# Performance work log

Measured on AMD Instinct MI355X. Metric: run time of the kernel, lower is better.

Reference implementation:

```python
import jax, jax.numpy as jnp
import numpy as np

NUM_HEADS = 8
NUM_GROUPS = 32
EPS = 1e-5


def setup_inputs() -> dict:
    key = jax.random.key(0)
    ks = jax.random.split(key, 6)
    C = 512
    scale = 1.0 / np.sqrt(C)
    return {
        "q": jax.random.normal(ks[0], (2, C, 64, 64), dtype=jnp.float32),
        "gn_w": jnp.ones((C,), jnp.float32),
        "gn_b": jnp.zeros((C,), jnp.float32),
        "wq": jax.random.normal(ks[1], (C, C), jnp.float32) * scale,
        "bq": jnp.zeros((C,), jnp.float32),
        "wk": jax.random.normal(ks[2], (C, C), jnp.float32) * scale,
        "bk": jnp.zeros((C,), jnp.float32),
        "wv": jax.random.normal(ks[3], (C, C), jnp.float32) * scale,
        "bv": jnp.zeros((C,), jnp.float32),
        "wo": jax.random.normal(ks[4], (C, C), jnp.float32) * scale,
        "bo": jnp.zeros((C,), jnp.float32),
    }


def _group_norm(x, w, b):
    # x: [B, C, H, W]
    B, C, H, W = x.shape
    xg = x.reshape(B, NUM_GROUPS, C // NUM_GROUPS, H, W)
    mean = xg.mean(axis=(2, 3, 4), keepdims=True)
    var = xg.var(axis=(2, 3, 4), keepdims=True)
    xn = ((xg - mean) * jax.lax.rsqrt(var + EPS)).reshape(B, C, H, W)
    return xn * w[None, :, None, None] + b[None, :, None, None]


def reference(q, gn_w, gn_b, wq, bq, wk, bk, wv, bv, wo, bo):
    B, C, H, W = q.shape
    hd = C // NUM_HEADS
    resid = q
    x = _group_norm(q, gn_w, gn_b)
    x = x.reshape(B, C, H * W).transpose(0, 2, 1)  # [B, N, C]
    # torch Linear: y = x @ W.T + b  (self-attention: k = v = x)
    qp = x @ wq.T + bq
    kp = x @ wk.T + bk
    vp = x @ wv.T + bv
    N = H * W
    def split(t):  # [B, N, C] -> [B, h, N, hd]
        return t.reshape(B, N, NUM_HEADS, hd).transpose(0, 2, 1, 3)
    qh, kh, vh = split(qp), split(kp), split(vp)
    scores = jnp.einsum('bhnc,bhmc->bhnm', qh, kh) / jnp.sqrt(jnp.float32(hd))
    attn = jax.nn.softmax(scores, axis=-1)
    out = jnp.einsum('bhnm,bhmc->bhnc', attn, vh)
    out = out.transpose(0, 2, 1, 3).reshape(B, N, C)
    out = out @ wo.T + bo
    out2d = out.transpose(0, 2, 1).reshape(B, C, H, W)
    return out2d + resid
```

## Files before the change

### kernel.cpp

```cpp
#include <hip/hip_runtime.h>
#include <hip/hip_bf16.h>
#include <cstdint>
#include <cstddef>

using bf16x8   = __attribute__((ext_vector_type(8))) short;
using f32x4    = __attribute__((ext_vector_type(4))) float;
using f32x16   = __attribute__((ext_vector_type(16))) float;
using ushort8  = __attribute__((ext_vector_type(8))) unsigned short;
using ushort4v = __attribute__((ext_vector_type(4))) unsigned short;
using float4v  = __attribute__((ext_vector_type(4))) float;

#define MFMA16(a,b,c) __builtin_amdgcn_mfma_f32_16x16x32_bf16((a),(b),(c),0,0,0)
#define MFMA32(a,b,c) __builtin_amdgcn_mfma_f32_32x32x16_bf16((a),(b),(c),0,0,0)

#define QSCALE 0.18033688011112042f

__device__ __forceinline__ unsigned short f2bf(float f){
    union { float f; unsigned u; } v; v.f = f;
    unsigned r = v.u + 0x7FFFu + ((v.u >> 16) & 1u);
    return (unsigned short)(r >> 16);
}

__device__ __forceinline__ int cvtpk(float lo, float hi){
    int r;
    asm volatile("v_cvt_pk_bf16_f32 %0, %1, %2" : "=v"(r) : "v"(lo), "v"(hi));
    return r;
}

#if __has_builtin(__builtin_amdgcn_permlane32_swap)
__device__ __forceinline__ void plswap(int &a, int &b){
    auto r = __builtin_amdgcn_permlane32_swap(a, b, false, false);
    a = r[0]; b = r[1];
}
#else
__device__ __forceinline__ void plswap(int &a, int &b){
    int ta = __shfl_xor(a, 32), tb = __shfl_xor(b, 32);
    bool hi = ((threadIdx.x & 63) >= 32);
    int na = hi ? tb : a;
    int nb = hi ? b  : ta;
    a = na; b = nb;
}
#endif

__device__ __forceinline__ void gload16(const unsigned short* g, unsigned short* l){
    __builtin_amdgcn_global_load_lds(
        (const __attribute__((address_space(1))) void*)g,
        (__attribute__((address_space(3))) void*)l,
        16, 0, 0);
}

__global__ __launch_bounds__(256) void gn_stats(const float* __restrict__ x,
                                                float* __restrict__ mean,
                                                float* __restrict__ rstd){
    int bg = blockIdx.x;
    const float4v* p4 = (const float4v*)(x + (size_t)bg * 65536);
    float s = 0.f, ss = 0.f;
    for (int i = threadIdx.x; i < 16384; i += 256){
        float4v v = p4[i];
        s  += v[0]+v[1]+v[2]+v[3];
        ss += v[0]*v[0]+v[1]*v[1]+v[2]*v[2]+v[3]*v[3];
    }
    __shared__ float ls[4], lss[4];
    int lane = threadIdx.x & 63, w = threadIdx.x >> 6;
    #pragma unroll
    for (int o = 32; o > 0; o >>= 1){ s += __shfl_down(s, o); ss += __shfl_down(ss, o); }
    if (lane == 0){ ls[w] = s; lss[w] = ss; }
    __syncthreads();
    if (threadIdx.x == 0){
        float S = ls[0]+ls[1]+ls[2]+ls[3];
        float SS = lss[0]+lss[1]+lss[2]+lss[3];
        float m = S * (1.f/65536.f);
        float var = SS * (1.f/65536.f) - m*m;
        mean[bg] = m;
        rstd[bg] = rsqrtf(var + 1e-5f);
    }
}

__global__ __launch_bounds__(256) void gn_apply(const float* __restrict__ x,
                                                const float* __restrict__ mean,
                                                const float* __restrict__ rstd,
                                                const float* __restrict__ gw,
                                                const float* __restrict__ gb,
                                                unsigned short* __restrict__ xn){
    int b = blockIdx.z, c0 = blockIdx.y * 64, n0 = blockIdx.x * 64;
    __shared__ unsigned short tile[64][68];
    for (int i = threadIdx.x; i < 64*16; i += 256){
        int row = i >> 4, f4 = i & 15;
        int c = c0 + row;
        int g = b*32 + (c >> 4);
        float rs = rstd[g];
        float wgt = gw[c] * rs;
        float bia = gb[c] - mean[g] * wgt;
        float4v v = *(const float4v*)(x + ((size_t)(b*512 + c))*4096 + n0 + f4*4);
        ushort4v o;
        #pragma unroll
        for (int j = 0; j < 4; j++) o[j] = f2bf(v[j]*wgt + bia);
        *(ushort4v*)&tile[row][f4*4] = o;
    }
    __syncthreads();
    for (int i = threadIdx.x; i < 64*8; i += 256){
        int nr = i >> 3, c8 = i & 7;
        ushort8 o;
        #pragma unroll
        for (int j = 0; j < 8; j++) o[j] = tile[c8*8 + j][nr];
        *(ushort8*)(xn + ((size_t)(b*4096 + n0 + nr))*512 + c0 + c8*8) = o;
    }
}

__global__ __launch_bounds__(256) void wconv(const float* __restrict__ w0, const float* __restrict__ w1,
                                             const float* __restrict__ w2, const float* __restrict__ w3,
                                             unsigned short* wqk, unsigned short* wv, unsigned short* wo){
    const float* src; unsigned short* dst; float sc = 1.0f;
    switch (blockIdx.y){
        case 0: src = w0; dst = wqk;          sc = QSCALE; break;
        case 1: src = w1; dst = wqk + 512*512; break;
        case 2: src = w2; dst = wv; break;
        default: src = w3; dst = wo; break;
    }
    int i = (blockIdx.x*256 + threadIdx.x) * 4;
    float4v v = *(const float4v*)(src + i);
    ushort4v o;
    #pragma unroll
    for (int j = 0; j < 4; j++) o[j] = f2bf(v[j]*sc);
    *(ushort4v*)(dst + i) = o;
}

__global__ __launch_bounds__(256) void gemm_qk2(const unsigned short* __restrict__ xn,
                                                const unsigned short* __restrict__ wqk,
                                                const float* __restrict__ bq,
                                                const float* __restrict__ bk,
                                                unsigned short* __restrict__ Q,
                                                unsigned short* __restrict__ K){
    __shared__ unsigned short Al[128*32];
    __shared__ unsigned short Bl[128*32];
    int t = threadIdx.x, lane = t & 63, w = t >> 6;
    int wr = w >> 1, wc = w & 1;
    int m0 = blockIdx.x * 128, n0 = blockIdx.y * 128;
    int lr = lane >> 2, lc = lane & 3;
    f32x4 acc[4][4] = {};

    const unsigned short* Asrc = xn  + (size_t)(m0 + w*32 + lr)*512 + lc*8;
    const unsigned short* Bsrc = wqk + (size_t)(n0 + w*32 + lr)*512 + lc*8;
    unsigned short* Adst = &Al[(w*32)*32];
    unsigned short* Bdst = &Bl[(w*32)*32];

    for (int ks = 0; ks < 16; ks++){
        gload16(Asrc + ks*32,          Adst);
        gload16(Asrc + ks*32 + 16*512, Adst + 16*32);
        gload16(Bsrc + ks*32,          Bdst);
        gload16(Bsrc + ks*32 + 16*512, Bdst + 16*32);
        asm volatile("s_waitcnt vmcnt(0)" ::: "memory");
        __syncthreads();
        bf16x8 a[4], b[4];
        #pragma unroll
        for (int mi = 0; mi < 4; mi++) a[mi] = *(bf16x8*)&Al[(wr*64 + mi*16 + (lane&15))*32 + (lane>>4)*8];
        #pragma unroll
        for (int ni = 0; ni < 4; ni++) b[ni] = *(bf16x8*)&Bl[(wc*64 + ni*16 + (lane&15))*32 + (lane>>4)*8];
        #pragma unroll
        for (int mi = 0; mi < 4; mi++)
            #pragma unroll
            for (int ni = 0; ni < 4; ni++)
                acc[mi][ni] = MFMA16(a[mi], b[ni], acc[mi][ni]);
        __syncthreads();
    }

    int cK = n0 >> 9;
    const float* bias = cK ? bk : bq;
    unsigned short* dst0 = cK ? K : Q;
    float bsc = cK ? 1.0f : QSCALE;
    #pragma unroll
    for (int mi = 0; mi < 4; mi++)
        #pragma unroll
        for (int ni = 0; ni < 4; ni++)
            #pragma unroll
            for (int r = 0; r < 4; r++){
                int mrow = m0 + wr*64 + mi*16 + (lane>>4)*4 + r;
                int col  = (n0 & 511) + wc*64 + ni*16 + (lane&15);
                int b_ = mrow >> 12, n = mrow & 4095;
                int h = col >> 6, d = col & 63;
                float v = acc[mi][ni][r] + bias[col]*bsc;
                dst0[(size_t)((b_*8+h)*4096 + n)*64 + d] = f2bf(v);
            }
}

__global__ __launch_bounds__(256) void gemm_v2(const unsigned short* __restrict__ Wv,
                                               const unsigned short* __restrict__ xn,
                                               const float* __restrict__ bv,
                                               unsigned short* __restrict__ Vt){
    __shared__ unsigned short Al[64*32];
    __shared__ unsigned short Bl[128*32];
    int t = threadIdx.x, lane = t & 63, w = t >> 6;
    int wr = w >> 1, wc = w & 1;
    int m0 = blockIdx.x * 64, n0 = blockIdx.y * 128;
    int lr = lane >> 2, lc = lane & 3;
    f32x4 acc[2][4] = {};

    const unsigned short* Asrc = Wv + (size_t)(m0 + w*16 + lr)*512 + lc*8;
    const unsigned short* Bsrc = xn + (size_t)(n0 + w*32 + lr)*512 + lc*8;
    unsigned short* Adst = &Al[(w*16)*32];
    unsigned short* Bdst = &Bl[(w*32)*32];

    for (int ks = 0; ks < 16; ks++){
        gload16(Asrc + ks*32,          Adst);
        gload16(Bsrc + ks*32,          Bdst);
        gload16(Bsrc + ks*32 + 16*512, Bdst + 16*32);
        asm volatile("s_waitcnt vmcnt(0)" ::: "memory");
        __syncthreads();
        bf16x8 a[2], b[4];
        #pragma unroll
        for (int mi = 0; mi < 2; mi++) a[mi] = *(bf16x8*)&Al[(wr*32 + mi*16 + (lane&15))*32 + (lane>>4)*8];
        #pragma unroll
        for (int ni = 0; ni < 4; ni++) b[ni] = *(bf16x8*)&Bl[(wc*64 + ni*16 + (lane&15))*32 + (lane>>4)*8];
        #pragma unroll
        for (int mi = 0; mi < 2; mi++)
            #pragma unroll
            for (int ni = 0; ni < 4; ni++)
                acc[mi][ni] = MFMA16(a[mi], b[ni], acc[mi][ni]);
        __syncthreads();
    }
    #pragma unroll
    for (int mi = 0; mi < 2; mi++)
        #pragma unroll
        for (int ni = 0; ni < 4; ni++)
            #pragma unroll
            for (int r = 0; r < 4; r++){
                int row  = m0 + wr*32 + mi*16 + (lane>>4)*4 + r;
                int colm = n0 + wc*64 + ni*16 + (lane&15);
                int b_ = colm >> 12, n = colm & 4095;
                int h = row >> 6, d = row & 63;
                float v = acc[mi][ni][r] + bv[row];
                Vt[(size_t)((b_*8+h)*64 + d)*4096 + n] = f2bf(v);
            }
}

__global__ __launch_bounds__(256) void gemm_o2(const unsigned short* __restrict__ Wo,
                                               const unsigned short* __restrict__ Om,
                                               const float* __restrict__ bo,
                                               const float* __restrict__ resid,
                                               float* __restrict__ outp){
    __shared__ unsigned short Al[64*32];
    __shared__ unsigned short Bl[128*32];
    int t = threadIdx.x, lane = t & 63, w = t >> 6;
    int wr = w >> 1, wc = w & 1;
    int m0 = blockIdx.x * 64, n0 = blockIdx.y * 128;
    int lr = lane >> 2, lc = lane & 3;
    f32x4 acc[2][4] = {};

    const unsigned short* Asrc = Wo + (size_t)(m0 + w*16 + lr)*512 + lc*8;
    const unsigned short* Bsrc = Om + (size_t)(n0 + w*32 + lr)*512 + lc*8;
    unsigned short* Adst = &Al[(w*16)*32];
    unsigned short* Bdst = &Bl[(w*32)*32];

    for (int ks = 0; ks < 16; ks++){
        gload16(Asrc + ks*32,          Adst);
        gload16(Bsrc + ks*32,          Bdst);
        gload16(Bsrc + ks*32 + 16*512, Bdst + 16*32);
        asm volatile("s_waitcnt vmcnt(0)" ::: "memory");
        __syncthreads();
        bf16x8 a[2], b[4];
        #pragma unroll
        for (int mi = 0; mi < 2; mi++) a[mi] = *(bf16x8*)&Al[(wr*32 + mi*16 + (lane&15))*32 + (lane>>4)*8];
        #pragma unroll
        for (int ni = 0; ni < 4; ni++) b[ni] = *(bf16x8*)&Bl[(wc*64 + ni*16 + (lane&15))*32 + (lane>>4)*8];
        #pragma unroll
        for (int mi = 0; mi < 2; mi++)
            #pragma unroll
            for (int ni = 0; ni < 4; ni++)
                acc[mi][ni] = MFMA16(a[mi], b[ni], acc[mi][ni]);
        __syncthreads();
    }
    #pragma unroll
    for (int mi = 0; mi < 2; mi++)
        #pragma unroll
        for (int ni = 0; ni < 4; ni++)
            #pragma unroll
            for (int r = 0; r < 4; r++){
                int row  = m0 + wr*32 + mi*16 + (lane>>4)*4 + r;
                int colm = n0 + wc*64 + ni*16 + (lane&15);
                int b_ = colm >> 12, n = colm & 4095;
                size_t oi = ((size_t)(b_*512 + row))*4096 + n;
                outp[oi] = acc[mi][ni][r] + bo[row] + resid[oi];
            }
}

__global__ __launch_bounds__(128, 2) void attn5(const unsigned short* __restrict__ Q,
                                                const unsigned short* __restrict__ K,
                                                const unsigned short* __restrict__ Vt,
                                                unsigned short* __restrict__ O){
    int bid = blockIdx.x;
    int idx = bid >> 3;
    int bh = ((bid & 7) << 1) | (idx >> 6);
    int qt = idx & 63;
    int t = threadIdx.x, lane = t & 63, w = t >> 6;
    int ln = lane & 31, hi = lane >> 5;
    int q0 = qt * 64;

    __shared__ unsigned short Kl[2][64*64];
    __shared__ unsigned short Vl[2][64*64];

    const unsigned short* Qb = Q  + (size_t)bh * 4096 * 64;
    const unsigned short* Kb = K  + (size_t)bh * 4096 * 64;
    const unsigned short* Vb = Vt + (size_t)bh * 64 * 4096;

    bf16x8 bqa[4], bqb[4];
    #pragma unroll
    for (int dsub = 0; dsub < 4; dsub++){
        bqa[dsub] = *(const bf16x8*)(Qb + (size_t)(q0 + ln)*64      + dsub*16 + hi*8);
        bqb[dsub] = *(const bf16x8*)(Qb + (size_t)(q0 + 32 + ln)*64 + dsub*16 + hi*8);
    }

    int srow = lane >> 3;
    int sswz = (lane & 7) ^ srow;

    auto stage = [&](int buf, int kt){
        int kv0 = kt * 64;
        #pragma unroll
        for (int i = 0; i < 4; i++){
            int r0 = w*32 + i*8;
            gload16(Kb + (size_t)(kv0 + r0 + srow)*64 + sswz*8, &Kl[buf][r0*64]);
        }
        #pragma unroll
        for (int i = 0; i < 4; i++){
            int r0 = w*32 + i*8;
            gload16(Vb + (size_t)(r0 + srow)*4096 + kv0 + sswz*8, &Vl[buf][r0*64]);
        }
    };

    stage(0, 0);

    f32x16 o0a, o1a, o0b, o1b, z;
    #pragma unroll
    for (int r = 0; r < 16; r++){ o0a[r]=0.f; o1a[r]=0.f; o0b[r]=0.f; o1b[r]=0.f; z[r]=0.f; }
    float lsA = 0.f, lsB = 0.f;

    const char* KbA = (const char*)&Kl[0][0] + (w*32 + ln)*128;
    const char* VbA = (const char*)&Vl[0][0] + ln*128;
    int swzr = (ln & 7) << 4;

    for (int kt = 0; kt < 64; kt++){
        asm volatile("s_waitcnt vmcnt(0)" ::: "memory");
        __builtin_amdgcn_s_barrier();
        __builtin_amdgcn_sched_barrier(0);
        if (kt < 63) stage((kt + 1) & 1, kt + 1);
        __builtin_amdgcn_sched_barrier(0);

        int boff = (kt & 1) * (64*64*2);

        f32x16 sA, sB;
        {
            int cb = (hi*16) ^ swzr;
            bf16x8 ak = *(const bf16x8*)(KbA + boff + cb);
            sA = MFMA32(ak, bqa[0], z);
            sB = MFMA32(ak, bqb[0], z);
        }
        __builtin_amdgcn_s_setprio(1);
        #pragma unroll
        for (int dsub = 1; dsub < 4; dsub++){
            int cb = (dsub*32 + hi*16) ^ swzr;
            bf16x8 ak = *(const bf16x8*)(KbA + boff + cb);
            sA = MFMA32(ak, bqa[dsub], sA);
            sB = MFMA32(ak, bqb[dsub], sB);
        }
        __builtin_amdgcn_s_setprio(0);

        #pragma unroll
        for (int r = 0; r < 16; r++){ sA[r] = __builtin_amdgcn_exp2f(sA[r]); lsA += sA[r]; }
        #pragma unroll
        for (int r = 0; r < 16; r++){ sB[r] = __builtin_amdgcn_exp2f(sB[r]); lsB += sB[r]; }

        __builtin_amdgcn_s_setprio(1);
        #pragma unroll
        for (int hsel = 0; hsel < 2; hsel++){
            int obp = hsel * 8;
            int a0 = cvtpk(sA[obp+0], sA[obp+1]);
            int a1 = cvtpk(sA[obp+2], sA[obp+3]);
            int c0 = cvtpk(sA[obp+4], sA[obp+5]);
            int c1 = cvtpk(sA[obp+6], sA[obp+7]);
            plswap(a0, c0);
            plswap(a1, c1);
            union { int i[4]; bf16x8 v; } fuA;
            fuA.i[0] = a0; fuA.i[1] = a1; fuA.i[2] = c0; fuA.i[3] = c1;

            int d0 = cvtpk(sB[obp+0], sB[obp+1]);
            int d1 = cvtpk(sB[obp+2], sB[obp+3]);
            int e0 = cvtpk(sB[obp+4], sB[obp+5]);
            int e1 = cvtpk(sB[obp+6], sB[obp+7]);
            plswap(d0, e0);
            plswap(d1, e1);
            union { int i[4]; bf16x8 v; } fuB;
            fuB.i[0] = d0; fuB.i[1] = d1; fuB.i[2] = e0; fuB.i[3] = e1;

            int cb = ((w*4 + hsel*2 + hi) << 4) ^ swzr;
            bf16x8 av0 = *(const bf16x8*)(VbA + boff + cb);
            bf16x8 av1 = *(const bf16x8*)(VbA + boff + 32*128 + cb);
            o0a = MFMA32(av0, fuA.v, o0a);
            o1a = MFMA32(av1, fuA.v, o1a);
            o0b = MFMA32(av0, fuB.v, o0b);
            o1b = MFMA32(av1, fuB.v, o1b);
        }
        __builtin_amdgcn_s_setprio(0);
    }

    lsA += __shfl_xor(lsA, 32);
    lsB += __shfl_xor(lsB, 32);
    __syncthreads();
    float* m1 = (float*)&Kl[0][0];
    float* m2 = (float*)&Vl[0][0];
    if (w == 1){
        #pragma unroll
        for (int r = 0; r < 16; r++){
            m1[r*64 + lane]        = o0a[r];
            m1[1024 + r*64 + lane] = o1a[r];
            m2[r*64 + lane]        = o0b[r];
            m2[1024 + r*64 + lane] = o1b[r];
        }
        if (hi == 0){ m2[2048 + ln] = lsA; m2[2048 + 32 + ln] = lsB; }
    }
    __syncthreads();
    if (w == 0){
        #pragma unroll
        for (int r = 0; r < 16; r++){
            o0a[r] += m1[r*64 + lane];
            o1a[r] += m1[1024 + r*64 + lane];
            o0b[r] += m2[r*64 + lane];
            o1b[r] += m2[1024 + r*64 + lane];
        }
        float rA = 1.0f / (lsA + m2[2048 + ln]);
        float rB = 1.0f / (lsB + m2[2048 + 32 + ln]);
        int b = bh >> 3, h = bh & 7;
        unsigned short* dstA = O + (size_t)(b*4096 + q0 + ln)*512      + h*64;
        unsigned short* dstB = O + (size_t)(b*4096 + q0 + 32 + ln)*512 + h*64;
        #pragma unroll
        for (int m = 0; m < 2; m++){
            const f32x16& ovA = m ? o1a : o0a;
            const f32x16& ovB = m ? o1b : o0b;
            #pragma unroll
            for (int g = 0; g < 4; g++){
                int d = m*32 + g*8 + hi*4;
                ushort4v pkA, pkB;
                #pragma unroll
                for (int j = 0; j < 4; j++){
                    pkA[j] = f2bf(ovA[g*4 + j] * rA);
                    pkB[j] = f2bf(ovB[g*4 + j] * rB);
                }
                *(ushort4v*)(dstA + d) = pkA;
                *(ushort4v*)(dstB + d) = pkB;
            }
        }
    }
}

extern "C" void kernel_launch(void* const* d_in, const int* in_sizes, int n_in,
                              void* d_out, int out_size, void* d_ws, size_t ws_size,
                              hipStream_t stream) {
    const float* q    = (const float*)d_in[0];
    const float* gn_w = (const float*)d_in[1];
    const float* gn_b = (const float*)d_in[2];
    const float* wq   = (const float*)d_in[3];
    const float* bq   = (const float*)d_in[4];
    const float* wk   = (const float*)d_in[5];
    const float* bk   = (const float*)d_in[6];
    const float* wv   = (const float*)d_in[7];
    const float* bv   = (const float*)d_in[8];
    const float* wo   = (const float*)d_in[9];
    const float* bo   = (const float*)d_in[10];
    float* outp = (float*)d_out;

    char* ws = (char*)d_ws;
    float* mean = (float*)ws;
    float* rstd = (float*)(ws + 256);
    unsigned short* xn  = (unsigned short*)(ws + 1024);
    const size_t TOK = (size_t)8192 * 512;
    unsigned short* wqkb = xn + TOK;
    unsigned short* wvb  = wqkb + 1024*512;
    unsigned short* wob  = wvb + 512*512;
    unsigned short* Qb   = wob + 512*512;
    unsigned short* Kb   = Qb + TOK;
    unsigned short* Vt   = Kb + TOK;
    unsigned short* Ob   = Vt + TOK;

    gn_stats<<<64, 256, 0, stream>>>(q, mean, rstd);
    gn_apply<<<dim3(64, 8, 2), 256, 0, stream>>>(q, mean, rstd, gn_w, gn_b, xn);
    wconv<<<dim3(256, 4), 256, 0, stream>>>(wq, wk, wv, wo, wqkb, wvb, wob);
    gemm_qk2<<<dim3(64, 8), 256, 0, stream>>>(xn, wqkb, bq, bk, Qb, Kb);
    gemm_v2<<<dim3(8, 64), 256, 0, stream>>>(wvb, xn, bv, Vt);
    attn5<<<1024, 128, 0, stream>>>(Qb, Kb, Vt, Ob);
    gemm_o2<<<dim3(8, 64), 256, 0, stream>>>(wob, Ob, bo, q, outp);
}
```

Baseline: 160.5 us.

## Software-pipeline attention: overlap next QK^T with softmax/PV, load V directly to registers

The attention kernel no longer stages V through LDS. Each lane loads its V fragments straight from global memory into registers one tile ahead. The loop is unrolled by two with ping-pong score registers, so the QK^T MFMAs for tile t+1 are issued before the exp/convert/PV work of tile t, and the barrier now waits with vmcnt(4) instead of draining all loads. This aims to hide MFMA and exp latency and halve LDS traffic and footprint, at the cost of more VGPRs (extra score and V registers) and uncoalesced-ish direct V global reads.

```diff
diff --git a/kernel.cpp b/kernel.cpp
--- a/kernel.cpp
+++ b/kernel.cpp
@@ -283,7 +283,7 @@
             }
 }
 
-__global__ __launch_bounds__(128, 2) void attn5(const unsigned short* __restrict__ Q,
+__global__ __launch_bounds__(128, 2) void attn6(const unsigned short* __restrict__ Q,
                                                 const unsigned short* __restrict__ K,
                                                 const unsigned short* __restrict__ Vt,
                                                 unsigned short* __restrict__ O){
@@ -291,12 +291,12 @@
     int idx = bid >> 3;
     int bh = ((bid & 7) << 1) | (idx >> 6);
     int qt = idx & 63;
-    int t = threadIdx.x, lane = t & 63, w = t >> 6;
+    int t_ = threadIdx.x, lane = t_ & 63, w = t_ >> 6;
     int ln = lane & 31, hi = lane >> 5;
     int q0 = qt * 64;
 
     __shared__ unsigned short Kl[2][64*64];
-    __shared__ unsigned short Vl[2][64*64];
+    __shared__ float mb[4224];
 
     const unsigned short* Qb = Q  + (size_t)bh * 4096 * 64;
     const unsigned short* Kb = K  + (size_t)bh * 4096 * 64;
@@ -312,121 +312,141 @@
     int srow = lane >> 3;
     int sswz = (lane & 7) ^ srow;
 
-    auto stage = [&](int buf, int kt){
+    auto stageK = [&](int kt){
         int kv0 = kt * 64;
+        unsigned short* dst = &Kl[kt & 1][0];
         #pragma unroll
         for (int i = 0; i < 4; i++){
             int r0 = w*32 + i*8;
-            gload16(Kb + (size_t)(kv0 + r0 + srow)*64 + sswz*8, &Kl[buf][r0*64]);
-        }
-        #pragma unroll
-        for (int i = 0; i < 4; i++){
-            int r0 = w*32 + i*8;
-            gload16(Vb + (size_t)(r0 + srow)*4096 + kv0 + sswz*8, &Vl[buf][r0*64]);
+            gload16(Kb + (size_t)(kv0 + r0 + srow)*64 + sswz*8, dst + r0*64);
         }
     };
 
-    stage(0, 0);
-
-    f32x16 o0a, o1a, o0b, o1b, z;
+    const unsigned short* Vbase = Vb + (size_t)ln*4096 + w*32 + hi*8;
+
+    f32x16 o0a, o1a, o0b, o1b, z, sEA, sEB, sOA, sOB;
     #pragma unroll
     for (int r = 0; r < 16; r++){ o0a[r]=0.f; o1a[r]=0.f; o0b[r]=0.f; o1b[r]=0.f; z[r]=0.f; }
     float lsA = 0.f, lsB = 0.f;
+    bf16x8 Ve0, Ve1, Ve2, Ve3, Vo0, Vo1, Vo2, Vo3;
 
     const char* KbA = (const char*)&Kl[0][0] + (w*32 + ln)*128;
-    const char* VbA = (const char*)&Vl[0][0] + ln*128;
     int swzr = (ln & 7) << 4;
 
-    for (int kt = 0; kt < 64; kt++){
-        asm volatile("s_waitcnt vmcnt(0)" ::: "memory");
-        __builtin_amdgcn_s_barrier();
+#define VLOAD(V0,V1,V2,V3, kt) { \
+    const unsigned short* vp = Vbase + (size_t)(kt)*64; \
+    V0 = *(const bf16x8*)(vp); \
+    V1 = *(const bf16x8*)(vp + (size_t)32*4096); \
+    V2 = *(const bf16x8*)(vp + 16); \
+    V3 = *(const bf16x8*)(vp + 16 + (size_t)32*4096); }
+
+#define QKSTEP(SA,SB, BOFF) { \
+    { int cb = (hi*16) ^ swzr; \
+      bf16x8 ak = *(const bf16x8*)(KbA + (BOFF) + cb); \
+      SA = MFMA32(ak, bqa[0], z); \
+      SB = MFMA32(ak, bqb[0], z); } \
+    _Pragma("unroll") \
+    for (int dsub = 1; dsub < 4; dsub++){ \
+        int cb = (dsub*32 + hi*16) ^ swzr; \
+        bf16x8 ak = *(const bf16x8*)(KbA + (BOFF) + cb); \
+        SA = MFMA32(ak, bqa[dsub], SA); \
+        SB = MFMA32(ak, bqb[dsub], SB); \
+    } }
+
+#define FINISH(SA,SB, V0,V1,V2,V3) { \
+    _Pragma("unroll") \
+    for (int r = 0; r < 16; r++){ SA[r] = __builtin_amdgcn_exp2f(SA[r]); lsA += SA[r]; } \
+    _Pragma("unroll") \
+    for (int r = 0; r < 16; r++){ SB[r] = __builtin_amdgcn_exp2f(SB[r]); lsB += SB[r]; } \
+    _Pragma("unroll") \
+    for (int hsel = 0; hsel < 2; hsel++){ \
+        int obp = hsel * 8; \
+        int a0 = cvtpk(SA[obp+0], SA[obp+1]); \
+        int a1 = cvtpk(SA[obp+2], SA[obp+3]); \
+        int c0 = cvtpk(SA[obp+4], SA[obp+5]); \
+        int c1 = cvtpk(SA[obp+6], SA[obp+7]); \
+        plswap(a0, c0); plswap(a1, c1); \
+        union { int i[4]; bf16x8 v; } fuA; \
+        fuA.i[0] = a0; fuA.i[1] = a1; fuA.i[2] = c0; fuA.i[3] = c1; \
+        int d0 = cvtpk(SB[obp+0], SB[obp+1]); \
+        int d1 = cvtpk(SB[obp+2], SB[obp+3]); \
+        int e0 = cvtpk(SB[obp+4], SB[obp+5]); \
+        int e1 = cvtpk(SB[obp+6], SB[obp+7]); \
+        plswap(d0, e0); plswap(d1, e1); \
+        union { int i[4]; bf16x8 v; } fuB; \
+        fuB.i[0] = d0; fuB.i[1] = d1; fuB.i[2] = e0; fuB.i[3] = e1; \
+        bf16x8 av0 = hsel ? V2 : V0; \
+        bf16x8 av1 = hsel ? V3 : V1; \
+        o0a = MFMA32(av0, fuA.v, o0a); \
+        o1a = MFMA32(av1, fuA.v, o1a); \
+        o0b = MFMA32(av0, fuB.v, o0b); \
+        o1b = MFMA32(av1, fuB.v, o1b); \
+    } }
+
+#define TILETOP() \
+    asm volatile("s_waitcnt vmcnt(4)" ::: "memory"); \
+    __builtin_amdgcn_s_barrier(); \
+    __builtin_amdgcn_sched_barrier(0);
+
+    stageK(0);
+    VLOAD(Ve0,Ve1,Ve2,Ve3, 0)
+
+    TILETOP()
+    stageK(1);
+    __builtin_amdgcn_sched_barrier(0);
+    QKSTEP(sEA, sEB, 0)
+    VLOAD(Vo0,Vo1,Vo2,Vo3, 1)
+
+    for (int tt = 0; tt < 31; tt++){
+        int t = 2*tt + 1;
+        TILETOP()
+        stageK(t + 1);
         __builtin_amdgcn_sched_barrier(0);
-        if (kt < 63) stage((kt + 1) & 1, kt + 1);
+        QKSTEP(sOA, sOB, 64*64*2)
+        FINISH(sEA, sEB, Ve0,Ve1,Ve2,Ve3)
+        VLOAD(Ve0,Ve1,Ve2,Ve3, t + 1)
+        TILETOP()
+        stageK(t + 2);
         __builtin_amdgcn_sched_barrier(0);
-
-        int boff = (kt & 1) * (64*64*2);
-
-        f32x16 sA, sB;
-        {
-            int cb = (hi*16) ^ swzr;
-            bf16x8 ak = *(const bf16x8*)(KbA + boff + cb);
-            sA = MFMA32(ak, bqa[0], z);
-            sB = MFMA32(ak, bqb[0], z);
-        }
-        __builtin_amdgcn_s_setprio(1);
-        #pragma unroll
-        for (int dsub = 1; dsub < 4; dsub++){
-            int cb = (dsub*32 + hi*16) ^ swzr;
-            bf16x8 ak = *(const bf16x8*)(KbA + boff + cb);
-            sA = MFMA32(ak, bqa[dsub], sA);
-            sB = MFMA32(ak, bqb[dsub], sB);
-        }
-        __builtin_amdgcn_s_setprio(0);
-
-        #pragma unroll
-        for (int r = 0; r < 16; r++){ sA[r] = __builtin_amdgcn_exp2f(sA[r]); lsA += sA[r]; }
-        #pragma unroll
-        for (int r = 0; r < 16; r++){ sB[r] = __builtin_amdgcn_exp2f(sB[r]); lsB += sB[r]; }
-
-        __builtin_amdgcn_s_setprio(1);
-        #pragma unroll
-        for (int hsel = 0; hsel < 2; hsel++){
-            int obp = hsel * 8;
-            int a0 = cvtpk(sA[obp+0], sA[obp+1]);
-            int a1 = cvtpk(sA[obp+2], sA[obp+3]);
-            int c0 = cvtpk(sA[obp+4], sA[obp+5]);
-            int c1 = cvtpk(sA[obp+6], sA[obp+7]);
-            plswap(a0, c0);
-            plswap(a1, c1);
-            union { int i[4]; bf16x8 v; } fuA;
-            fuA.i[0] = a0; fuA.i[1] = a1; fuA.i[2] = c0; fuA.i[3] = c1;
-
-            int d0 = cvtpk(sB[obp+0], sB[obp+1]);
-            int d1 = cvtpk(sB[obp+2], sB[obp+3]);
-            int e0 = cvtpk(sB[obp+4], sB[obp+5]);
-            int e1 = cvtpk(sB[obp+6], sB[obp+7]);
-            plswap(d0, e0);
-            plswap(d1, e1);
-            union { int i[4]; bf16x8 v; } fuB;
-            fuB.i[0] = d0; fuB.i[1] = d1; fuB.i[2] = e0; fuB.i[3] = e1;
-
-            int cb = ((w*4 + hsel*2 + hi) << 4) ^ swzr;
-            bf16x8 av0 = *(const bf16x8*)(VbA + boff + cb);
-            bf16x8 av1 = *(const bf16x8*)(VbA + boff + 32*128 + cb);
-            o0a = MFMA32(av0, fuA.v, o0a);
-            o1a = MFMA32(av1, fuA.v, o1a);
-            o0b = MFMA32(av0, fuB.v, o0b);
-            o1b = MFMA32(av1, fuB.v, o1b);
-        }
-        __builtin_amdgcn_s_setprio(0);
-    }
+        QKSTEP(sEA, sEB, 0)
+        FINISH(sOA, sOB, Vo0,Vo1,Vo2,Vo3)
+        VLOAD(Vo0,Vo1,Vo2,Vo3, t + 2)
+    }
+
+    TILETOP()
+    QKSTEP(sOA, sOB, 64*64*2)
+    FINISH(sEA, sEB, Ve0,Ve1,Ve2,Ve3)
+    FINISH(sOA, sOB, Vo0,Vo1,Vo2,Vo3)
+
+#undef VLOAD
+#undef QKSTEP
+#undef FINISH
+#undef TILETOP
 
     lsA += __shfl_xor(lsA, 32);
     lsB += __shfl_xor(lsB, 32);
     __syncthreads();
-    float* m1 = (float*)&Kl[0][0];
-    float* m2 = (float*)&Vl[0][0];
     if (w == 1){
         #pragma unroll
         for (int r = 0; r < 16; r++){
-            m1[r*64 + lane]        = o0a[r];
-            m1[1024 + r*64 + lane] = o1a[r];
-            m2[r*64 + lane]        = o0b[r];
-            m2[1024 + r*64 + lane] = o1b[r];
+            mb[r*64 + lane]        = o0a[r];
+            mb[1024 + r*64 + lane] = o1a[r];
+            mb[2048 + r*64 + lane] = o0b[r];
+            mb[3072 + r*64 + lane] = o1b[r];
         }
-        if (hi == 0){ m2[2048 + ln] = lsA; m2[2048 + 32 + ln] = lsB; }
+        if (hi == 0){ mb[4096 + ln] = lsA; mb[4096 + 32 + ln] = lsB; }
     }
     __syncthreads();
     if (w == 0){
         #pragma unroll
         for (int r = 0; r < 16; r++){
-            o0a[r] += m1[r*64 + lane];
-            o1a[r] += m1[1024 + r*64 + lane];
-            o0b[r] += m2[r*64 + lane];
-            o1b[r] += m2[1024 + r*64 + lane];
+            o0a[r] += mb[r*64 + lane];
+            o1a[r] += mb[1024 + r*64 + lane];
+            o0b[r] += mb[2048 + r*64 + lane];
+            o1b[r] += mb[3072 + r*64 + lane];
         }
-        float rA = 1.0f / (lsA + m2[2048 + ln]);
-        float rB = 1.0f / (lsB + m2[2048 + 32 + ln]);
+        float rA = 1.0f / (lsA + mb[4096 + ln]);
+        float rB = 1.0f / (lsB + mb[4096 + 32 + ln]);
         int b = bh >> 3, h = bh & 7;
         unsigned short* dstA = O + (size_t)(b*4096 + q0 + ln)*512      + h*64;
         unsigned short* dstB = O + (size_t)(b*4096 + q0 + 32 + ln)*512 + h*64;
@@ -484,6 +504,6 @@
     wconv<<<dim3(256, 4), 256, 0, stream>>>(wq, wk, wv, wo, wqkb, wvb, wob);
     gemm_qk2<<<dim3(64, 8), 256, 0, stream>>>(xn, wqkb, bq, bk, Qb, Kb);
     gemm_v2<<<dim3(8, 64), 256, 0, stream>>>(wvb, xn, bv, Vt);
-    attn5<<<1024, 128, 0, stream>>>(Qb, Kb, Vt, Ob);
+    attn6<<<1024, 128, 0, stream>>>(Qb, Kb, Vt, Ob);
     gemm_o2<<<dim3(8, 64), 256, 0, stream>>>(wob, Ob, bo, q, outp);
 }
```

New measurement: 184.8 us. 15.1% more time.
